# Kernel tuning notes

Measured on AMD Instinct MI355X. Metric: run time of the kernel, lower is better.

The kernel has to match this reference:

```python
import jax, jax.numpy as jnp
import numpy as np

PNUM = 128
BATCH = 8192


def setup_inputs() -> dict:
    key = jax.random.key(0)
    k0, k1, k2 = jax.random.split(key, 3)
    return {
        "pred0": jax.random.normal(k0, (BATCH, PNUM, 2), dtype=jnp.float32),
        "pred1": jax.random.normal(k1, (BATCH, PNUM, 2), dtype=jnp.float32),
        "gt": jax.random.normal(k2, (BATCH, PNUM, 2), dtype=jnp.float32),
    }


def _smooth_l1(d):
    # F.smooth_l1_loss with default beta=1.0, reduction='none'
    a = jnp.abs(d)
    return jnp.where(a < 1.0, 0.5 * d * d, a - 0.5)


def _match_loss(pred, gt):
    # pred, gt: [B, pnum, 2]
    pnum = pred.shape[1]
    # cyclic index: idx[i, j] = (i + j) % pnum  (row i = gt rolled by i)
    idx = (jnp.arange(pnum)[:, None] + jnp.arange(pnum)[None, :]) % pnum
    gt_expand = gt[:, idx]                      # [B, pnum, pnum, 2]
    diff = pred[:, None, :, :] - gt_expand      # broadcast pred over shift dim i
    dis = _smooth_l1(diff).sum(-1).mean(axis=2)  # [B, pnum] mean over vertices j
    return jnp.min(dis, axis=1)                  # min over cyclic shift i -> [B]


def reference(pred0, pred1, gt):
    loss = _match_loss(pred0, gt).mean() + _match_loss(pred1, gt).mean()
    return loss / 2.0
```

## Files before the change

### kernel.cpp

```cpp
#include <hip/hip_runtime.h>

#define PNUM 128
#define BATCH 8192
#define NPAIR (2 * BATCH)
#define WPB 4
#define GRID1 (BATCH / WPB)

__device__ __forceinline__ float term(float p, float q, float acc) {
    float d = p - q;
    float m = fminf(fabsf(d), 1.0f);
    float t = fmaf(-0.5f, m, fabsf(d));
    return fmaf(m, t, acc);
}

__global__ __launch_bounds__(64 * WPB) void match_stage1(
        const float* __restrict__ pred0,
        const float* __restrict__ pred1,
        const float* __restrict__ gt,
        float* __restrict__ ws) {
    __shared__ float4 sg4[WPB][2 * PNUM / 2];

    const int t = threadIdx.x;
    const int k = t & 63;
    const int w = __builtin_amdgcn_readfirstlane(t >> 6);
    const int b = blockIdx.x * WPB + w;

    const float4* gv4 = (const float4*)(gt + (size_t)b * (PNUM * 2));
    float4 gA = gv4[k];
    sg4[w][k]      = gA;
    sg4[w][k + 64] = gA;

    const float4* gw4 = sg4[w];
    const float4* p0v = (const float4*)(pred0 + (size_t)b * (PNUM * 2));
    const float4* p1v = (const float4*)(pred1 + (size_t)b * (PNUM * 2));

    float4 w01 = gw4[k];
    float4 P0 = p0v[0], P1 = p1v[0];

    float a0p0 = 0.f, a1p0 = 0.f, a0p1 = 0.f, a1p1 = 0.f;

#pragma unroll 8
    for (int h = 0; h < PNUM / 2; ++h) {
        float4 n01 = gw4[k + h + 1];
        int hn = (h + 1) & 63;
        float4 P0n = p0v[hn];
        float4 P1n = p1v[hn];

        a0p0 = term(P0.x, w01.x, a0p0); a0p0 = term(P0.y, w01.y, a0p0);
        a0p0 = term(P0.z, w01.z, a0p0); a0p0 = term(P0.w, w01.w, a0p0);
        a0p1 = term(P1.x, w01.x, a0p1); a0p1 = term(P1.y, w01.y, a0p1);
        a0p1 = term(P1.z, w01.z, a0p1); a0p1 = term(P1.w, w01.w, a0p1);
        a1p0 = term(P0.x, w01.z, a1p0); a1p0 = term(P0.y, w01.w, a1p0);
        a1p0 = term(P0.z, n01.x, a1p0); a1p0 = term(P0.w, n01.y, a1p0);
        a1p1 = term(P1.x, w01.z, a1p1); a1p1 = term(P1.y, w01.w, a1p1);
        a1p1 = term(P1.z, n01.x, a1p1); a1p1 = term(P1.w, n01.y, a1p1);

        w01 = n01; P0 = P0n; P1 = P1n;
    }

    float r0 = fminf(a0p0, a1p0);
    float r1 = fminf(a0p1, a1p1);
#pragma unroll
    for (int m = 32; m > 0; m >>= 1) {
        r0 = fminf(r0, __shfl_xor(r0, m, 64));
        r1 = fminf(r1, __shfl_xor(r1, m, 64));
    }
    if (k == 0) {
        ws[2 * b]     = r0;
        ws[2 * b + 1] = r1;
    }
}

__global__ __launch_bounds__(1024) void match_stage2(
        const float* __restrict__ ws, float* __restrict__ out) {
    const int t = threadIdx.x;
    const float4* ws4 = (const float4*)ws;
    float s = 0.f;
#pragma unroll
    for (int q = 0; q < 4; ++q) {
        float4 v = ws4[t + q * 1024];
        s += (v.x + v.y) + (v.z + v.w);
    }
#pragma unroll
    for (int m = 32; m > 0; m >>= 1) s += __shfl_xor(s, m, 64);

    __shared__ float wsum[16];
    if ((t & 63) == 0) wsum[t >> 6] = s;
    __syncthreads();
    if (t == 0) {
        float tot = 0.f;
#pragma unroll
        for (int i = 0; i < 16; ++i) tot += wsum[i];
        out[0] = tot * (1.0f / (2.0f * BATCH * PNUM));
    }
}

extern "C" void kernel_launch(void* const* d_in, const int* in_sizes, int n_in,
                              void* d_out, int out_size, void* d_ws, size_t ws_size,
                              hipStream_t stream) {
    const float* pred0 = (const float*)d_in[0];
    const float* pred1 = (const float*)d_in[1];
    const float* gt    = (const float*)d_in[2];
    float* out = (float*)d_out;
    float* ws  = (float*)d_ws;

    match_stage1<<<GRID1, 64 * WPB, 0, stream>>>(pred0, pred1, gt, ws);
    match_stage2<<<1, 1024, 0, stream>>>(ws, out);
}
```

Before: 128.8 us.

## Fuse reduction into main kernel via last-block atomic counter and stage preds in LDS

Merges the two-kernel pipeline into one kernel. Each block writes a partial sum, and the last block to arrive, detected with an atomic counter, performs the final reduction. The per-iteration broadcast global loads of pred0/pred1 are replaced by staging them in shared memory first. Block size is halved to two waves with an occupancy hint. A memset is added to reset the counter, which adds a small launch, while the second kernel launch is removed.

```diff
diff --git a/kernel.cpp b/kernel.cpp
--- a/kernel.cpp
+++ b/kernel.cpp
@@ -2,49 +2,54 @@
 
 #define PNUM 128
 #define BATCH 8192
-#define NPAIR (2 * BATCH)
-#define WPB 4
+#define WPB 2
 #define GRID1 (BATCH / WPB)
 
 __device__ __forceinline__ float term(float p, float q, float acc) {
     float d = p - q;
-    float m = fminf(fabsf(d), 1.0f);
-    float t = fmaf(-0.5f, m, fabsf(d));
+    float a = fabsf(d);
+    float m = fminf(a, 1.0f);
+    float t = fmaf(-0.5f, m, a);
     return fmaf(m, t, acc);
 }
 
-__global__ __launch_bounds__(64 * WPB) void match_stage1(
+__global__ __launch_bounds__(64 * WPB, 8) void match_fused(
         const float* __restrict__ pred0,
         const float* __restrict__ pred1,
         const float* __restrict__ gt,
-        float* __restrict__ ws) {
-    __shared__ float4 sg4[WPB][2 * PNUM / 2];
+        unsigned* __restrict__ counter,
+        float* __restrict__ sums,
+        float* __restrict__ out) {
+    __shared__ float4 sg [WPB][2 * PNUM / 2];
+    __shared__ float4 sp0[WPB][PNUM / 2];
+    __shared__ float4 sp1[WPB][PNUM / 2];
 
     const int t = threadIdx.x;
     const int k = t & 63;
     const int w = __builtin_amdgcn_readfirstlane(t >> 6);
     const int b = blockIdx.x * WPB + w;
 
-    const float4* gv4 = (const float4*)(gt + (size_t)b * (PNUM * 2));
-    float4 gA = gv4[k];
-    sg4[w][k]      = gA;
-    sg4[w][k + 64] = gA;
-
-    const float4* gw4 = sg4[w];
+    const float4* gv4 = (const float4*)(gt    + (size_t)b * (PNUM * 2));
     const float4* p0v = (const float4*)(pred0 + (size_t)b * (PNUM * 2));
     const float4* p1v = (const float4*)(pred1 + (size_t)b * (PNUM * 2));
+    float4 gA = gv4[k];
+    sg[w][k]      = gA;
+    sg[w][k + 64] = gA;
+    sp0[w][k] = p0v[k];
+    sp1[w][k] = p1v[k];
+
+    const float4* gw4 = sg[w];
+    const float4* q0  = sp0[w];
+    const float4* q1  = sp1[w];
 
     float4 w01 = gw4[k];
-    float4 P0 = p0v[0], P1 = p1v[0];
-
     float a0p0 = 0.f, a1p0 = 0.f, a0p1 = 0.f, a1p1 = 0.f;
 
 #pragma unroll 8
     for (int h = 0; h < PNUM / 2; ++h) {
         float4 n01 = gw4[k + h + 1];
-        int hn = (h + 1) & 63;
-        float4 P0n = p0v[hn];
-        float4 P1n = p1v[hn];
+        float4 P0  = q0[h];
+        float4 P1  = q1[h];
 
         a0p0 = term(P0.x, w01.x, a0p0); a0p0 = term(P0.y, w01.y, a0p0);
         a0p0 = term(P0.z, w01.z, a0p0); a0p0 = term(P0.w, w01.w, a0p0);
@@ -55,7 +60,7 @@
         a1p1 = term(P1.x, w01.z, a1p1); a1p1 = term(P1.y, w01.w, a1p1);
         a1p1 = term(P1.z, n01.x, a1p1); a1p1 = term(P1.w, n01.y, a1p1);
 
-        w01 = n01; P0 = P0n; P1 = P1n;
+        w01 = n01;
     }
 
     float r0 = fminf(a0p0, a1p0);
@@ -65,33 +70,32 @@
         r0 = fminf(r0, __shfl_xor(r0, m, 64));
         r1 = fminf(r1, __shfl_xor(r1, m, 64));
     }
-    if (k == 0) {
-        ws[2 * b]     = r0;
-        ws[2 * b + 1] = r1;
-    }
-}
 
-__global__ __launch_bounds__(1024) void match_stage2(
-        const float* __restrict__ ws, float* __restrict__ out) {
-    const int t = threadIdx.x;
-    const float4* ws4 = (const float4*)ws;
-    float s = 0.f;
-#pragma unroll
-    for (int q = 0; q < 4; ++q) {
-        float4 v = ws4[t + q * 1024];
-        s += (v.x + v.y) + (v.z + v.w);
-    }
-#pragma unroll
-    for (int m = 32; m > 0; m >>= 1) s += __shfl_xor(s, m, 64);
-
-    __shared__ float wsum[16];
-    if ((t & 63) == 0) wsum[t >> 6] = s;
+    __shared__ float bsum[WPB];
+    __shared__ int isLast;
+    if (k == 0) bsum[w] = r0 + r1;
     __syncthreads();
     if (t == 0) {
-        float tot = 0.f;
+        sums[blockIdx.x] = bsum[0] + bsum[1];
+        __threadfence();
+        unsigned old = atomicAdd(counter, 1u);
+        isLast = (old == GRID1 - 1);
+    }
+    __syncthreads();
+    if (isLast) {
+        __threadfence();
+        float s = 0.f;
 #pragma unroll
-        for (int i = 0; i < 16; ++i) tot += wsum[i];
-        out[0] = tot * (1.0f / (2.0f * BATCH * PNUM));
+        for (int q = 0; q < GRID1 / 128; ++q)
+            s += sums[t + q * 128];
+#pragma unroll
+        for (int m = 32; m > 0; m >>= 1) s += __shfl_xor(s, m, 64);
+        __shared__ float wsum[WPB];
+        if (k == 0) wsum[w] = s;
+        __syncthreads();
+        if (t == 0) {
+            out[0] = (wsum[0] + wsum[1]) * (1.0f / (2.0f * BATCH * PNUM));
+        }
     }
 }
 
@@ -102,8 +106,10 @@
     const float* pred1 = (const float*)d_in[1];
     const float* gt    = (const float*)d_in[2];
     float* out = (float*)d_out;
-    float* ws  = (float*)d_ws;
+    unsigned* counter = (unsigned*)d_ws;
+    float* sums = (float*)d_ws + 16;
 
-    match_stage1<<<GRID1, 64 * WPB, 0, stream>>>(pred0, pred1, gt, ws);
-    match_stage2<<<1, 1024, 0, stream>>>(ws, out);
+    hipMemsetAsync(d_ws, 0, 64, stream);
+    match_fused<<<GRID1, 64 * WPB, 0, stream>>>(pred0, pred1, gt,
+                                                counter, sums, out);
 }
```

Result: slower. 217.3 us (+68.7%).
